# Optimization experiments

Hardware: AMD Instinct MI355X
Metric: run time of the kernel (lower is better)

Reference implementation:

```python
import jax, jax.numpy as jnp
import numpy as np

N, D, V, T = 1024, 64, 32000, 2048
U_DECAY = 0.97
LN_EPS = 1e-6


def _layernorm_row(z):
    # matches torch: (z - mean) / (std_unbiased + eps), std uses ddof=1
    m = z.mean(axis=-1, keepdims=True)
    s = jnp.std(z, axis=-1, ddof=1, keepdims=True)
    return (z - m) / (s + LN_EPS)


def setup_inputs() -> dict:
    key = jax.random.key(0)
    k1, k2, k3, k4, k5 = jax.random.split(key, 5)
    E = jax.random.normal(k1, (D, N), dtype=jnp.float32) / np.float32(np.sqrt(N))
    Dx = jax.random.normal(k2, (N, D), dtype=jnp.float32) / np.float32(np.sqrt(D))
    Dy = jax.random.normal(k3, (N, D), dtype=jnp.float32) / np.float32(np.sqrt(D))
    token_emb = jax.random.normal(k4, (V, D), dtype=jnp.float32) / np.float32(np.sqrt(D))
    tokens = jax.random.randint(k5, (T,), 0, V, dtype=jnp.int32)
    x0 = jnp.zeros((N,), dtype=jnp.float32)
    rho0 = jnp.zeros((D, N), dtype=jnp.float32)
    return {"E": E, "Dx": Dx, "Dy": Dy, "token_emb": token_emb,
            "x0": x0, "rho0": rho0, "tokens": tokens}


def reference(E, Dx, Dy, token_emb, x0, rho0, tokens):
    def step(carry, tok):
        x, rho = carry                        # x: [N], rho: [D, N]
        v_prev = token_emb[tok]               # [D]
        x_t = x + jax.nn.relu(Dx @ v_prev)    # [N], use_relu_lowrank=True
        a_star = rho @ x_t                    # [D]
        y_core = Dy @ _layernorm_row(a_star)  # ln_before_Dy=True -> [N]
        y_t = jax.nn.relu(y_core) * jax.nn.relu(x_t)  # [N]
        v_star = _layernorm_row(E @ y_t)      # [D]
        rho_new = U_DECAY * (rho + jnp.outer(v_prev, x_t))  # [D, N]
        return (x_t, rho_new), (y_t, v_star)

    (_, _), (ys, vs) = jax.lax.scan(step, (x0, rho0), tokens)
    return ys, vs  # [T, N], [T, D]
```

## Files before the change

kernel.cpp:

```cpp
#include <hip/hip_runtime.h>
#include <math.h>

#define NN 1024
#define DD 64
#define TT 2048
#define UDEC 0.97f
#define EPS 1e-6f
#define CC 64
#define NCH 32
#define NSL 8
#define SLW 128
#define C2 32
#define NC2 64

__global__ __launch_bounds__(256) void k_xscan(
    const float* __restrict__ Dx, const float* __restrict__ temb,
    const int* __restrict__ toks, float* __restrict__ Xp, float* __restrict__ S)
{
    const int cs = blockIdx.y;
    const int n  = blockIdx.x * 256 + threadIdx.x;
    __shared__ float Vs[C2][DD];
    for (int i = threadIdx.x; i < C2 * DD; i += 256) {
        int s = i >> 6, d = i & 63;
        Vs[s][d] = temb[toks[cs * C2 + s] * DD + d];
    }
    __syncthreads();
    float dxr[DD];
    const float4* dx4 = reinterpret_cast<const float4*>(Dx + n * DD);
#pragma unroll
    for (int j = 0; j < DD / 4; ++j) {
        float4 v = dx4[j];
        dxr[4*j] = v.x; dxr[4*j+1] = v.y; dxr[4*j+2] = v.z; dxr[4*j+3] = v.w;
    }
    float run = 0.f;
    for (int s = 0; s < C2; ++s) {
        const float4* vr = reinterpret_cast<const float4*>(&Vs[s][0]);
        float a0 = 0.f, a1 = 0.f, a2 = 0.f, a3 = 0.f;
#pragma unroll
        for (int j = 0; j < DD / 4; ++j) {
            float4 v = vr[j];
            a0 += v.x * dxr[4*j];     a1 += v.y * dxr[4*j+1];
            a2 += v.z * dxr[4*j+2];   a3 += v.w * dxr[4*j+3];
        }
        float r = (a0 + a1) + (a2 + a3);
        run += fmaxf(r, 0.f);
        Xp[(cs * C2 + s) * NN + n] = run;
    }
    S[cs * NN + n] = run;
}

__global__ __launch_bounds__(256) void k_base(
    const float* __restrict__ S, const float* __restrict__ x0, float* __restrict__ Bb)
{
    const int n = blockIdx.x * 256 + threadIdx.x;
    float acc = x0[n];
    for (int cs = 0; cs < NC2; ++cs) {
        Bb[cs * NN + n] = acc;
        acc += S[cs * NN + n];
    }
}


__global__ __launch_bounds__(256) void k_M(
    const float* __restrict__ Xp, const float* __restrict__ Bb,
    const float* __restrict__ temb, const int* __restrict__ toks, float* __restrict__ M)
{
    const int c = blockIdx.y, q = blockIdx.x;
    __shared__ float Xs[CC][SLW + 1];
    __shared__ float Vw[CC][DD];
    __shared__ float pw[CC + 1];
    const int tid = threadIdx.x;
    if (tid <= CC) pw[tid] = powf(UDEC, (float)tid);
    __syncthreads();
    for (int i = tid; i < CC * SLW; i += 256) {
        int s = i / SLW, n = i % SLW;
        int t = c * CC + s, gn = q * SLW + n;
        Xs[s][n] = Xp[t * NN + gn] + Bb[(t >> 5) * NN + gn];
    }
    for (int i = tid; i < CC * DD; i += 256) {
        int s = i >> 6, d = i & 63;
        Vw[s][d] = temb[toks[c * CC + s] * DD + d] * pw[CC - s];
    }
    __syncthreads();
    const int n_l = tid & 127;
    const int dh  = tid >> 7;
    float acc[32];
#pragma unroll
    for (int k = 0; k < 32; ++k) acc[k] = 0.f;
    for (int s = 0; s < CC; ++s) {
        float xv = Xs[s][n_l];
        const float4* vr = reinterpret_cast<const float4*>(&Vw[s][dh * 32]);
#pragma unroll
        for (int k8 = 0; k8 < 8; ++k8) {
            float4 v = vr[k8];
            acc[4*k8]   += v.x * xv;  acc[4*k8+1] += v.y * xv;
            acc[4*k8+2] += v.z * xv;  acc[4*k8+3] += v.w * xv;
        }
    }
    for (int k = 0; k < 32; ++k)
        M[(c * DD + dh * 32 + k) * NN + q * SLW + n_l] = acc[k];
}

__global__ __launch_bounds__(256) void k_rho(
    const float* __restrict__ M, const float* __restrict__ rho0, float* __restrict__ Rho)
{
    const int el = blockIdx.x * 256 + threadIdx.x;
    float acc = rho0[el];
    const float uc = powf(UDEC, (float)CC);
    for (int c = 0; c < NCH; ++c) {
        Rho[c * (DD * NN) + el] = acc;
        acc = fmaf(acc, uc, M[c * (DD * NN) + el]);
    }
}

__global__ __launch_bounds__(256) void k_gram(
    const float* __restrict__ Xp, const float* __restrict__ Bb,
    const float* __restrict__ Rho, float* __restrict__ Gp, float* __restrict__ Pp)
{
    const int c = blockIdx.y, q = blockIdx.x;
    __shared__ float Xs[CC][SLW + 1];
    __shared__ float Rs[DD][SLW + 1];
    const int tid = threadIdx.x;
    for (int i = tid; i < CC * SLW; i += 256) {
        int s = i / SLW, n = i % SLW;
        int t = c * CC + s, gn = q * SLW + n;
        Xs[s][n] = Xp[t * NN + gn] + Bb[(t >> 5) * NN + gn];
        Rs[s][n] = Rho[(c * DD + s) * NN + gn];
    }
    __syncthreads();
    const int ti = tid >> 4;
    const int sj = tid & 15;
    float acc[16];
#pragma unroll
    for (int k = 0; k < 16; ++k) acc[k] = 0.f;
    for (int n = 0; n < SLW; ++n) {
        float xt[4], xs[4];
#pragma unroll
        for (int a = 0; a < 4; ++a) xt[a] = Xs[ti * 4 + a][n];
#pragma unroll
        for (int b = 0; b < 4; ++b) xs[b] = Xs[sj * 4 + b][n];
#pragma unroll
        for (int a = 0; a < 4; ++a)
#pragma unroll
            for (int b = 0; b < 4; ++b) acc[a * 4 + b] += xt[a] * xs[b];
    }
    {
        float* base = Gp + ((size_t)(c * NSL + q) * CC) * CC;
#pragma unroll
        for (int a = 0; a < 4; ++a)
            *reinterpret_cast<float4*>(base + (ti * 4 + a) * CC + sj * 4) =
                make_float4(acc[a*4], acc[a*4+1], acc[a*4+2], acc[a*4+3]);
    }
#pragma unroll
    for (int k = 0; k < 16; ++k) acc[k] = 0.f;
    for (int n = 0; n < SLW; ++n) {
        float xt[4], rv[4];
#pragma unroll
        for (int a = 0; a < 4; ++a) xt[a] = Xs[ti * 4 + a][n];
#pragma unroll
        for (int b = 0; b < 4; ++b) rv[b] = Rs[sj * 4 + b][n];
#pragma unroll
        for (int a = 0; a < 4; ++a)
#pragma unroll
            for (int b = 0; b < 4; ++b) acc[a * 4 + b] += xt[a] * rv[b];
    }
    {
        float* base = Pp + ((size_t)(c * NSL + q) * CC) * DD;
#pragma unroll
        for (int a = 0; a < 4; ++a)
            *reinterpret_cast<float4*>(base + (ti * 4 + a) * DD + sj * 4) =
                make_float4(acc[a*4], acc[a*4+1], acc[a*4+2], acc[a*4+3]);
    }
}

__global__ __launch_bounds__(256) void k_astar(
    const float* __restrict__ Gp, const float* __restrict__ Pp,
    const float* __restrict__ temb, const int* __restrict__ toks,
    float* __restrict__ LNA)
{
    const int c = blockIdx.x;
    __shared__ float G[CC][CC + 1];
    __shared__ float P[CC][DD + 1];
    __shared__ float Ve[CC][DD];
    __shared__ float As[CC][DD + 1];
    __shared__ float pw[CC + 1];
    __shared__ float mrow[CC], srow[CC];
    const int tid = threadIdx.x;
    if (tid <= CC) pw[tid] = powf(UDEC, (float)tid);
    for (int i = tid; i < CC * CC; i += 256) {
        int t = i >> 6, s = i & 63;
        float ag = 0.f, ap = 0.f;
#pragma unroll
        for (int qq = 0; qq < NSL; ++qq) {
            ag += Gp[((size_t)(c * NSL + qq) * CC + t) * CC + s];
            ap += Pp[((size_t)(c * NSL + qq) * CC + t) * DD + s];
        }
        G[t][s] = ag; P[t][s] = ap;
    }
    for (int i = tid; i < CC * DD; i += 256) {
        int s = i >> 6, d = i & 63;
        Ve[s][d] = temb[toks[c * CC + s] * DD + d];
    }
    __syncthreads();
    const int t_l = tid >> 2;
    const int qq  = tid & 3;
    float acc[16];
#pragma unroll
    for (int j = 0; j < 16; ++j) acc[j] = pw[t_l] * P[t_l][qq * 16 + j];
    for (int s = 0; s < t_l; ++s) {
        float wv = pw[t_l - s] * G[t_l][s];
        const float4* ver = reinterpret_cast<const float4*>(&Ve[s][qq * 16]);
#pragma unroll
        for (int k = 0; k < 4; ++k) {
            float4 v = ver[k];
            acc[4*k]   += wv * v.x;  acc[4*k+1] += wv * v.y;
            acc[4*k+2] += wv * v.z;  acc[4*k+3] += wv * v.w;
        }
    }
#pragma unroll
    for (int j = 0; j < 16; ++j) As[t_l][qq * 16 + j] = acc[j];
    __syncthreads();
    if (tid < CC) {
        float m = 0.f;
#pragma unroll
        for (int d = 0; d < DD; ++d) m += As[tid][d];
        m *= (1.f / DD);
        float v = 0.f;
#pragma unroll
        for (int d = 0; d < DD; ++d) { float z = As[tid][d] - m; v += z * z; }
        mrow[tid] = m;
        srow[tid] = 1.f / (sqrtf(v / (DD - 1)) + EPS);
    }
    __syncthreads();
    for (int i = tid; i < CC * DD; i += 256) {
        int t = i >> 6, d = i & 63;
        LNA[(c * CC + t) * DD + d] = (As[t][d] - mrow[t]) * srow[t];
    }
}

__global__ __launch_bounds__(256) void k_y(
    const float* __restrict__ LNA, const float* __restrict__ Dy,
    const float* __restrict__ Xp, const float* __restrict__ Bb,
    float* __restrict__ ys)
{
    const int tt = blockIdx.y;
    const int n  = blockIdx.x * 256 + threadIdx.x;
    __shared__ float L[8][DD];
    for (int i = threadIdx.x; i < 8 * DD; i += 256) L[i >> 6][i & 63] = LNA[tt * 8 * DD + i];
    __syncthreads();
    float dyr[DD];
    const float4* dy4 = reinterpret_cast<const float4*>(Dy + n * DD);
#pragma unroll
    for (int j = 0; j < 16; ++j) {
        float4 v = dy4[j];
        dyr[4*j] = v.x; dyr[4*j+1] = v.y; dyr[4*j+2] = v.z; dyr[4*j+3] = v.w;
    }
#pragma unroll
    for (int t = 0; t < 8; ++t) {
        const float4* lr = reinterpret_cast<const float4*>(&L[t][0]);
        float a0 = 0.f, a1 = 0.f, a2 = 0.f, a3 = 0.f;
#pragma unroll
        for (int j = 0; j < 16; ++j) {
            float4 v = lr[j];
            a0 += v.x * dyr[4*j];   a1 += v.y * dyr[4*j+1];
            a2 += v.z * dyr[4*j+2]; a3 += v.w * dyr[4*j+3];
        }
        float yc = (a0 + a1) + (a2 + a3);
        int tg = tt * 8 + t;
        float xv = Xp[tg * NN + n] + Bb[(tg >> 5) * NN + n];
        ys[tg * NN + n] = fmaxf(yc, 0.f) * fmaxf(xv, 0.f);
    }
}

__global__ __launch_bounds__(256) void k_v(
    const float* __restrict__ ys, const float* __restrict__ E, float* __restrict__ vs)
{
    const int tt = blockIdx.x;
    __shared__ float Ys[8][NN];
    __shared__ float pre[8][DD + 1];
    __shared__ float mrow[8], srow[8];
    const int tid = threadIdx.x;
    for (int i = tid; i < 8 * NN; i += 256) Ys[i >> 10][i & 1023] = ys[tt * 8 * NN + i];
    __syncthreads();
    const int d  = tid & 63;
    const int tq = tid >> 6;
    const int t0 = tq * 2;
    const float4* e4 = reinterpret_cast<const float4*>(E + d * NN);
    float a00=0,a01=0,a02=0,a03=0, a10=0,a11=0,a12=0,a13=0;
    for (int j = 0; j < NN / 4; ++j) {
        float4 ev  = e4[j];
        float4 y0v = *reinterpret_cast<const float4*>(&Ys[t0][4 * j]);
        float4 y1v = *reinterpret_cast<const float4*>(&Ys[t0 + 1][4 * j]);
        a00 += ev.x * y0v.x; a01 += ev.y * y0v.y; a02 += ev.z * y0v.z; a03 += ev.w * y0v.w;
        a10 += ev.x * y1v.x; a11 += ev.y * y1v.y; a12 += ev.z * y1v.z; a13 += ev.w * y1v.w;
    }
    pre[t0][d]     = (a00 + a01) + (a02 + a03);
    pre[t0 + 1][d] = (a10 + a11) + (a12 + a13);
    __syncthreads();
    if (tid < 8) {
        float m = 0.f;
#pragma unroll
        for (int dd2 = 0; dd2 < DD; ++dd2) m += pre[tid][dd2];
        m *= (1.f / DD);
        float v = 0.f;
#pragma unroll
        for (int dd2 = 0; dd2 < DD; ++dd2) { float z = pre[tid][dd2] - m; v += z * z; }
        mrow[tid] = m;
        srow[tid] = 1.f / (sqrtf(v / (DD - 1)) + EPS);
    }
    __syncthreads();
    for (int i = tid; i < 8 * DD; i += 256) {
        int t = i >> 6, dd2 = i & 63;
        vs[(tt * 8 + t) * DD + dd2] = (pre[t][dd2] - mrow[t]) * srow[t];
    }
}

extern "C" void kernel_launch(void* const* d_in, const int* in_sizes, int n_in,
                              void* d_out, int out_size, void* d_ws, size_t ws_size,
                              hipStream_t stream) {
    (void)in_sizes; (void)n_in; (void)out_size; (void)ws_size;
    const float* E    = (const float*)d_in[0];
    const float* Dx   = (const float*)d_in[1];
    const float* Dy   = (const float*)d_in[2];
    const float* temb = (const float*)d_in[3];
    const float* x0   = (const float*)d_in[4];
    const float* rho0 = (const float*)d_in[5];
    const int*   toks = (const int*)d_in[6];

    float* ys = (float*)d_out;
    float* vs = ys + (size_t)TT * NN;

    float* w   = (float*)d_ws;
    float* Xp  = w;
    float* S   = Xp  + (size_t)TT * NN;
    float* Bb  = S   + (size_t)NC2 * NN;
    float* M   = Bb  + (size_t)NC2 * NN;
    float* Rho = M   + (size_t)NCH * DD * NN;
    float* LNA = Rho + (size_t)NCH * DD * NN;
    float* Gp = M;
    float* Pp = M + (size_t)NCH * NSL * CC * CC;

    k_xscan<<<dim3(4, NC2),  256, 0, stream>>>(Dx, temb, toks, Xp, S);
    k_base <<<dim3(4),       256, 0, stream>>>(S, x0, Bb);
    k_M    <<<dim3(NSL, NCH),256, 0, stream>>>(Xp, Bb, temb, toks, M);
    k_rho  <<<dim3(DD*NN/256),256,0, stream>>>(M, rho0, Rho);
    k_gram <<<dim3(NSL, NCH),256, 0, stream>>>(Xp, Bb, Rho, Gp, Pp);
    k_astar<<<dim3(NCH),     256, 0, stream>>>(Gp, Pp, temb, toks, LNA);
    k_y    <<<dim3(4, TT/8), 256, 0, stream>>>(LNA, Dy, Xp, Bb, ys);
    k_v    <<<dim3(TT/8),    256, 0, stream>>>(ys, E, vs);
}
```

Baseline: 193.4 us.

## Fuse all phases into one cooperative persistent kernel with grid syncs

Replaces the eight separate kernel launches with one cooperative kernel of 256 blocks that runs each phase in turn, separated by grid-wide barriers. The y and v computations are fused so ys stays in shared memory, the gram phase is split into finer slices with the G and P accumulations merged into one loop, and the a* LayerNorm now uses wave shuffles spread over more blocks. A fallback path launches the phases as separate kernels if the cooperative launch fails. This removes launch gaps and the ys re-read, at the cost of grid.sync overhead and a unified shared-memory footprint that may lower occupancy.

```diff
diff --git a/kernel.cpp b/kernel.cpp
--- a/kernel.cpp
+++ b/kernel.cpp
@@ -1,5 +1,8 @@
 #include <hip/hip_runtime.h>
+#include <hip/hip_cooperative_groups.h>
 #include <math.h>
+
+namespace cg = cooperative_groups;
 
 #define NN 1024
 #define DD 64
@@ -8,78 +11,78 @@
 #define EPS 1e-6f
 #define CC 64
 #define NCH 32
-#define NSL 8
-#define SLW 128
+#define SL3 128
+#define NS5 16
+#define SL5 64
 #define C2 32
 #define NC2 64
 
-__global__ __launch_bounds__(256) void k_xscan(
-    const float* __restrict__ Dx, const float* __restrict__ temb,
-    const int* __restrict__ toks, float* __restrict__ Xp, float* __restrict__ S)
-{
-    const int cs = blockIdx.y;
-    const int n  = blockIdx.x * 256 + threadIdx.x;
-    __shared__ float Vs[C2][DD];
-    for (int i = threadIdx.x; i < C2 * DD; i += 256) {
+struct SP1 { float Vs[C2][DD]; };
+struct SP3 { float Xs[CC][SL3 + 1]; float Vw[CC][DD]; float pw[CC + 1]; };
+struct SP5 { float Xs[CC][SL5 + 1]; float Rs[CC][SL5 + 1]; };
+struct SP6 { float Gs[8][CC + 1]; float Ps[8][DD]; float Ve[CC][DD]; float pw[CC + 1]; };
+struct SP7 { float L[8][DD]; float Ys[8][NN]; float pre[8][DD + 1]; float mrow[8]; float srow[8]; };
+union SMem { SP1 p1; SP3 p3; SP5 p5; SP6 p6; SP7 p7; };
+
+struct KP {
+    const float *E, *Dx, *Dy, *temb, *x0, *rho0;
+    const int* toks;
+    float *ys, *vs;
+    float *Xp, *S, *Bb, *M, *Rho, *Gp, *Pp, *LNA;
+};
+
+__device__ __forceinline__ void phase1(const KP& p, SMem& sm, int bid, int tid) {
+    const int cs = bid >> 2;
+    const int n  = (bid & 3) * 256 + tid;
+    for (int i = tid; i < C2 * DD; i += 256) {
         int s = i >> 6, d = i & 63;
-        Vs[s][d] = temb[toks[cs * C2 + s] * DD + d];
+        sm.p1.Vs[s][d] = p.temb[p.toks[cs * C2 + s] * DD + d];
     }
     __syncthreads();
     float dxr[DD];
-    const float4* dx4 = reinterpret_cast<const float4*>(Dx + n * DD);
-#pragma unroll
-    for (int j = 0; j < DD / 4; ++j) {
+    const float4* dx4 = reinterpret_cast<const float4*>(p.Dx + n * DD);
+#pragma unroll
+    for (int j = 0; j < 16; ++j) {
         float4 v = dx4[j];
         dxr[4*j] = v.x; dxr[4*j+1] = v.y; dxr[4*j+2] = v.z; dxr[4*j+3] = v.w;
     }
     float run = 0.f;
     for (int s = 0; s < C2; ++s) {
-        const float4* vr = reinterpret_cast<const float4*>(&Vs[s][0]);
+        const float4* vr = reinterpret_cast<const float4*>(&sm.p1.Vs[s][0]);
         float a0 = 0.f, a1 = 0.f, a2 = 0.f, a3 = 0.f;
 #pragma unroll
-        for (int j = 0; j < DD / 4; ++j) {
+        for (int j = 0; j < 16; ++j) {
             float4 v = vr[j];
-            a0 += v.x * dxr[4*j];     a1 += v.y * dxr[4*j+1];
-            a2 += v.z * dxr[4*j+2];   a3 += v.w * dxr[4*j+3];
-        }
-        float r = (a0 + a1) + (a2 + a3);
-        run += fmaxf(r, 0.f);
-        Xp[(cs * C2 + s) * NN + n] = run;
-    }
-    S[cs * NN + n] = run;
-}
-
-__global__ __launch_bounds__(256) void k_base(
-    const float* __restrict__ S, const float* __restrict__ x0, float* __restrict__ Bb)
-{
-    const int n = blockIdx.x * 256 + threadIdx.x;
-    float acc = x0[n];
+            a0 += v.x * dxr[4*j];   a1 += v.y * dxr[4*j+1];
+            a2 += v.z * dxr[4*j+2]; a3 += v.w * dxr[4*j+3];
+        }
+        run += fmaxf((a0 + a1) + (a2 + a3), 0.f);
+        p.Xp[(cs * C2 + s) * NN + n] = run;
+    }
+    p.S[cs * NN + n] = run;
+}
+
+__device__ __forceinline__ void phase2(const KP& p, int bid, int tid) {
+    const int n = bid * 256 + tid;
+    float acc = p.x0[n];
     for (int cs = 0; cs < NC2; ++cs) {
-        Bb[cs * NN + n] = acc;
-        acc += S[cs * NN + n];
-    }
-}
-
-
-__global__ __launch_bounds__(256) void k_M(
-    const float* __restrict__ Xp, const float* __restrict__ Bb,
-    const float* __restrict__ temb, const int* __restrict__ toks, float* __restrict__ M)
-{
-    const int c = blockIdx.y, q = blockIdx.x;
-    __shared__ float Xs[CC][SLW + 1];
-    __shared__ float Vw[CC][DD];
-    __shared__ float pw[CC + 1];
-    const int tid = threadIdx.x;
-    if (tid <= CC) pw[tid] = powf(UDEC, (float)tid);
-    __syncthreads();
-    for (int i = tid; i < CC * SLW; i += 256) {
-        int s = i / SLW, n = i % SLW;
-        int t = c * CC + s, gn = q * SLW + n;
-        Xs[s][n] = Xp[t * NN + gn] + Bb[(t >> 5) * NN + gn];
+        p.Bb[cs * NN + n] = acc;
+        acc += p.S[cs * NN + n];
+    }
+}
+
+__device__ __forceinline__ void phase3(const KP& p, SMem& sm, int bid, int tid) {
+    const int c = bid >> 3, q = bid & 7;
+    if (tid <= CC) sm.p3.pw[tid] = powf(UDEC, (float)tid);
+    __syncthreads();
+    for (int i = tid; i < CC * SL3; i += 256) {
+        int s = i / SL3, n = i % SL3;
+        int t = c * CC + s, gn = q * SL3 + n;
+        sm.p3.Xs[s][n] = p.Xp[t * NN + gn] + p.Bb[(t >> 5) * NN + gn];
     }
     for (int i = tid; i < CC * DD; i += 256) {
         int s = i >> 6, d = i & 63;
-        Vw[s][d] = temb[toks[c * CC + s] * DD + d] * pw[CC - s];
+        sm.p3.Vw[s][d] = p.temb[p.toks[c * CC + s] * DD + d] * sm.p3.pw[CC - s];
     }
     __syncthreads();
     const int n_l = tid & 127;
@@ -88,8 +91,8 @@
 #pragma unroll
     for (int k = 0; k < 32; ++k) acc[k] = 0.f;
     for (int s = 0; s < CC; ++s) {
-        float xv = Xs[s][n_l];
-        const float4* vr = reinterpret_cast<const float4*>(&Vw[s][dh * 32]);
+        float xv = sm.p3.Xs[s][n_l];
+        const float4* vr = reinterpret_cast<const float4*>(&sm.p3.Vw[s][dh * 32]);
 #pragma unroll
         for (int k8 = 0; k8 < 8; ++k8) {
             float4 v = vr[k8];
@@ -98,254 +101,234 @@
         }
     }
     for (int k = 0; k < 32; ++k)
-        M[(c * DD + dh * 32 + k) * NN + q * SLW + n_l] = acc[k];
-}
-
-__global__ __launch_bounds__(256) void k_rho(
-    const float* __restrict__ M, const float* __restrict__ rho0, float* __restrict__ Rho)
-{
-    const int el = blockIdx.x * 256 + threadIdx.x;
-    float acc = rho0[el];
+        p.M[(c * DD + dh * 32 + k) * NN + q * SL3 + n_l] = acc[k];
+}
+
+__device__ __forceinline__ void phase4(const KP& p, int bid, int tid) {
+    const int el = bid * 256 + tid;
     const float uc = powf(UDEC, (float)CC);
+    float acc = p.rho0[el];
+#pragma unroll
     for (int c = 0; c < NCH; ++c) {
-        Rho[c * (DD * NN) + el] = acc;
-        acc = fmaf(acc, uc, M[c * (DD * NN) + el]);
-    }
-}
-
-__global__ __launch_bounds__(256) void k_gram(
-    const float* __restrict__ Xp, const float* __restrict__ Bb,
-    const float* __restrict__ Rho, float* __restrict__ Gp, float* __restrict__ Pp)
-{
-    const int c = blockIdx.y, q = blockIdx.x;
-    __shared__ float Xs[CC][SLW + 1];
-    __shared__ float Rs[DD][SLW + 1];
-    const int tid = threadIdx.x;
-    for (int i = tid; i < CC * SLW; i += 256) {
-        int s = i / SLW, n = i % SLW;
-        int t = c * CC + s, gn = q * SLW + n;
-        Xs[s][n] = Xp[t * NN + gn] + Bb[(t >> 5) * NN + gn];
-        Rs[s][n] = Rho[(c * DD + s) * NN + gn];
+        p.Rho[c * (DD * NN) + el] = acc;
+        acc = fmaf(acc, uc, p.M[c * (DD * NN) + el]);
+    }
+}
+
+__device__ __forceinline__ void phase5(const KP& p, SMem& sm, int work, int tid) {
+    const int c = work >> 4, q = work & 15;
+    for (int i = tid; i < CC * SL5; i += 256) {
+        int s = i >> 6, n = i & 63;
+        int t = c * CC + s, gn = q * SL5 + n;
+        sm.p5.Xs[s][n] = p.Xp[t * NN + gn] + p.Bb[(t >> 5) * NN + gn];
+        sm.p5.Rs[s][n] = p.Rho[(c * DD + s) * NN + gn];
     }
     __syncthreads();
     const int ti = tid >> 4;
     const int sj = tid & 15;
-    float acc[16];
-#pragma unroll
-    for (int k = 0; k < 16; ++k) acc[k] = 0.f;
-    for (int n = 0; n < SLW; ++n) {
-        float xt[4], xs[4];
-#pragma unroll
-        for (int a = 0; a < 4; ++a) xt[a] = Xs[ti * 4 + a][n];
-#pragma unroll
-        for (int b = 0; b < 4; ++b) xs[b] = Xs[sj * 4 + b][n];
+    float accG[16], accP[16];
+#pragma unroll
+    for (int k = 0; k < 16; ++k) { accG[k] = 0.f; accP[k] = 0.f; }
+    for (int n = 0; n < SL5; ++n) {
+        float xt[4], xs[4], rv[4];
+#pragma unroll
+        for (int a = 0; a < 4; ++a) xt[a] = sm.p5.Xs[ti * 4 + a][n];
+#pragma unroll
+        for (int b = 0; b < 4; ++b) { xs[b] = sm.p5.Xs[sj * 4 + b][n]; rv[b] = sm.p5.Rs[sj * 4 + b][n]; }
 #pragma unroll
         for (int a = 0; a < 4; ++a)
 #pragma unroll
-            for (int b = 0; b < 4; ++b) acc[a * 4 + b] += xt[a] * xs[b];
-    }
-    {
-        float* base = Gp + ((size_t)(c * NSL + q) * CC) * CC;
-#pragma unroll
-        for (int a = 0; a < 4; ++a)
-            *reinterpret_cast<float4*>(base + (ti * 4 + a) * CC + sj * 4) =
-                make_float4(acc[a*4], acc[a*4+1], acc[a*4+2], acc[a*4+3]);
-    }
-#pragma unroll
-    for (int k = 0; k < 16; ++k) acc[k] = 0.f;
-    for (int n = 0; n < SLW; ++n) {
-        float xt[4], rv[4];
-#pragma unroll
-        for (int a = 0; a < 4; ++a) xt[a] = Xs[ti * 4 + a][n];
-#pragma unroll
-        for (int b = 0; b < 4; ++b) rv[b] = Rs[sj * 4 + b][n];
-#pragma unroll
-        for (int a = 0; a < 4; ++a)
-#pragma unroll
-            for (int b = 0; b < 4; ++b) acc[a * 4 + b] += xt[a] * rv[b];
-    }
-    {
-        float* base = Pp + ((size_t)(c * NSL + q) * CC) * DD;
-#pragma unroll
-        for (int a = 0; a < 4; ++a)
-            *reinterpret_cast<float4*>(base + (ti * 4 + a) * DD + sj * 4) =
-                make_float4(acc[a*4], acc[a*4+1], acc[a*4+2], acc[a*4+3]);
-    }
-}
-
-__global__ __launch_bounds__(256) void k_astar(
-    const float* __restrict__ Gp, const float* __restrict__ Pp,
-    const float* __restrict__ temb, const int* __restrict__ toks,
-    float* __restrict__ LNA)
-{
-    const int c = blockIdx.x;
-    __shared__ float G[CC][CC + 1];
-    __shared__ float P[CC][DD + 1];
-    __shared__ float Ve[CC][DD];
-    __shared__ float As[CC][DD + 1];
-    __shared__ float pw[CC + 1];
-    __shared__ float mrow[CC], srow[CC];
-    const int tid = threadIdx.x;
-    if (tid <= CC) pw[tid] = powf(UDEC, (float)tid);
-    for (int i = tid; i < CC * CC; i += 256) {
-        int t = i >> 6, s = i & 63;
+            for (int b = 0; b < 4; ++b) {
+                accG[a * 4 + b] += xt[a] * xs[b];
+                accP[a * 4 + b] += xt[a] * rv[b];
+            }
+    }
+    float* gbase = p.Gp + ((size_t)(c * NS5 + q) * CC) * CC;
+    float* pbase = p.Pp + ((size_t)(c * NS5 + q) * CC) * DD;
+#pragma unroll
+    for (int a = 0; a < 4; ++a) {
+        *reinterpret_cast<float4*>(gbase + (ti * 4 + a) * CC + sj * 4) =
+            make_float4(accG[a*4], accG[a*4+1], accG[a*4+2], accG[a*4+3]);
+        *reinterpret_cast<float4*>(pbase + (ti * 4 + a) * DD + sj * 4) =
+            make_float4(accP[a*4], accP[a*4+1], accP[a*4+2], accP[a*4+3]);
+    }
+}
+
+__device__ __forceinline__ void phase6(const KP& p, SMem& sm, int bid, int tid) {
+    const int c = bid >> 3, rg = bid & 7;
+    if (tid <= CC) sm.p6.pw[tid] = powf(UDEC, (float)tid);
+    for (int i = tid; i < 8 * CC; i += 256) {
+        int r = i >> 6, s2 = i & 63;
+        int t = rg * 8 + r;
         float ag = 0.f, ap = 0.f;
 #pragma unroll
-        for (int qq = 0; qq < NSL; ++qq) {
-            ag += Gp[((size_t)(c * NSL + qq) * CC + t) * CC + s];
-            ap += Pp[((size_t)(c * NSL + qq) * CC + t) * DD + s];
-        }
-        G[t][s] = ag; P[t][s] = ap;
+        for (int qq = 0; qq < NS5; ++qq) {
+            ag += p.Gp[((size_t)(c * NS5 + qq) * CC + t) * CC + s2];
+            ap += p.Pp[((size_t)(c * NS5 + qq) * CC + t) * DD + s2];
+        }
+        sm.p6.Gs[r][s2] = ag;
+        sm.p6.Ps[r][s2] = ap;
     }
     for (int i = tid; i < CC * DD; i += 256) {
-        int s = i >> 6, d = i & 63;
-        Ve[s][d] = temb[toks[c * CC + s] * DD + d];
-    }
-    __syncthreads();
-    const int t_l = tid >> 2;
-    const int qq  = tid & 3;
-    float acc[16];
-#pragma unroll
-    for (int j = 0; j < 16; ++j) acc[j] = pw[t_l] * P[t_l][qq * 16 + j];
-    for (int s = 0; s < t_l; ++s) {
-        float wv = pw[t_l - s] * G[t_l][s];
-        const float4* ver = reinterpret_cast<const float4*>(&Ve[s][qq * 16]);
-#pragma unroll
-        for (int k = 0; k < 4; ++k) {
-            float4 v = ver[k];
-            acc[4*k]   += wv * v.x;  acc[4*k+1] += wv * v.y;
-            acc[4*k+2] += wv * v.z;  acc[4*k+3] += wv * v.w;
-        }
-    }
-#pragma unroll
-    for (int j = 0; j < 16; ++j) As[t_l][qq * 16 + j] = acc[j];
-    __syncthreads();
-    if (tid < CC) {
-        float m = 0.f;
-#pragma unroll
-        for (int d = 0; d < DD; ++d) m += As[tid][d];
-        m *= (1.f / DD);
-        float v = 0.f;
-#pragma unroll
-        for (int d = 0; d < DD; ++d) { float z = As[tid][d] - m; v += z * z; }
-        mrow[tid] = m;
-        srow[tid] = 1.f / (sqrtf(v / (DD - 1)) + EPS);
-    }
-    __syncthreads();
-    for (int i = tid; i < CC * DD; i += 256) {
-        int t = i >> 6, d = i & 63;
-        LNA[(c * CC + t) * DD + d] = (As[t][d] - mrow[t]) * srow[t];
-    }
-}
-
-__global__ __launch_bounds__(256) void k_y(
-    const float* __restrict__ LNA, const float* __restrict__ Dy,
-    const float* __restrict__ Xp, const float* __restrict__ Bb,
-    float* __restrict__ ys)
-{
-    const int tt = blockIdx.y;
-    const int n  = blockIdx.x * 256 + threadIdx.x;
-    __shared__ float L[8][DD];
-    for (int i = threadIdx.x; i < 8 * DD; i += 256) L[i >> 6][i & 63] = LNA[tt * 8 * DD + i];
-    __syncthreads();
-    float dyr[DD];
-    const float4* dy4 = reinterpret_cast<const float4*>(Dy + n * DD);
-#pragma unroll
-    for (int j = 0; j < 16; ++j) {
-        float4 v = dy4[j];
-        dyr[4*j] = v.x; dyr[4*j+1] = v.y; dyr[4*j+2] = v.z; dyr[4*j+3] = v.w;
-    }
-#pragma unroll
-    for (int t = 0; t < 8; ++t) {
-        const float4* lr = reinterpret_cast<const float4*>(&L[t][0]);
-        float a0 = 0.f, a1 = 0.f, a2 = 0.f, a3 = 0.f;
+        int s2 = i >> 6, d = i & 63;
+        sm.p6.Ve[s2][d] = p.temb[p.toks[c * CC + s2] * DD + d];
+    }
+    __syncthreads();
+    const int r   = tid >> 5;
+    const int dh  = tid & 31;
+    const int t_l = rg * 8 + r;
+    float a0 = sm.p6.pw[t_l] * sm.p6.Ps[r][2 * dh];
+    float a1 = sm.p6.pw[t_l] * sm.p6.Ps[r][2 * dh + 1];
+    for (int s2 = 0; s2 < t_l; ++s2) {
+        float w = sm.p6.pw[t_l - s2] * sm.p6.Gs[r][s2];
+        a0 += w * sm.p6.Ve[s2][2 * dh];
+        a1 += w * sm.p6.Ve[s2][2 * dh + 1];
+    }
+    float ssum = a0 + a1;
+#pragma unroll
+    for (int m = 16; m >= 1; m >>= 1) ssum += __shfl_xor(ssum, m, 64);
+    float mean = ssum * (1.f / DD);
+    float z0 = a0 - mean, z1 = a1 - mean;
+    float vsum = z0 * z0 + z1 * z1;
+#pragma unroll
+    for (int m = 16; m >= 1; m >>= 1) vsum += __shfl_xor(vsum, m, 64);
+    float inv = 1.f / (sqrtf(vsum * (1.f / (DD - 1))) + EPS);
+    int t = c * CC + t_l;
+    *reinterpret_cast<float2*>(&p.LNA[t * DD + 2 * dh]) = make_float2(z0 * inv, z1 * inv);
+}
+
+__device__ __forceinline__ void phase7(const KP& p, SMem& sm, int bid, int tid) {
+    const int t0 = bid * 8;
+    for (int i = tid; i < 8 * DD; i += 256)
+        sm.p7.L[i >> 6][i & 63] = p.LNA[t0 * DD + i];
+    __syncthreads();
+    for (int nq = 0; nq < 4; ++nq) {
+        const int n = nq * 256 + tid;
+        float dyr[DD];
+        const float4* dy4 = reinterpret_cast<const float4*>(p.Dy + n * DD);
 #pragma unroll
         for (int j = 0; j < 16; ++j) {
-            float4 v = lr[j];
-            a0 += v.x * dyr[4*j];   a1 += v.y * dyr[4*j+1];
-            a2 += v.z * dyr[4*j+2]; a3 += v.w * dyr[4*j+3];
-        }
-        float yc = (a0 + a1) + (a2 + a3);
-        int tg = tt * 8 + t;
-        float xv = Xp[tg * NN + n] + Bb[(tg >> 5) * NN + n];
-        ys[tg * NN + n] = fmaxf(yc, 0.f) * fmaxf(xv, 0.f);
-    }
-}
-
-__global__ __launch_bounds__(256) void k_v(
-    const float* __restrict__ ys, const float* __restrict__ E, float* __restrict__ vs)
-{
-    const int tt = blockIdx.x;
-    __shared__ float Ys[8][NN];
-    __shared__ float pre[8][DD + 1];
-    __shared__ float mrow[8], srow[8];
-    const int tid = threadIdx.x;
-    for (int i = tid; i < 8 * NN; i += 256) Ys[i >> 10][i & 1023] = ys[tt * 8 * NN + i];
+            float4 v = dy4[j];
+            dyr[4*j] = v.x; dyr[4*j+1] = v.y; dyr[4*j+2] = v.z; dyr[4*j+3] = v.w;
+        }
+#pragma unroll
+        for (int r = 0; r < 8; ++r) {
+            const float4* lr = reinterpret_cast<const float4*>(&sm.p7.L[r][0]);
+            float a0 = 0.f, a1 = 0.f, a2 = 0.f, a3 = 0.f;
+#pragma unroll
+            for (int j = 0; j < 16; ++j) {
+                float4 v = lr[j];
+                a0 += v.x * dyr[4*j];   a1 += v.y * dyr[4*j+1];
+                a2 += v.z * dyr[4*j+2]; a3 += v.w * dyr[4*j+3];
+            }
+            float yc = (a0 + a1) + (a2 + a3);
+            int t = t0 + r;
+            float xv = p.Xp[t * NN + n] + p.Bb[(t >> 5) * NN + n];
+            float yv = fmaxf(yc, 0.f) * fmaxf(xv, 0.f);
+            p.ys[t * NN + n] = yv;
+            sm.p7.Ys[r][n] = yv;
+        }
+    }
     __syncthreads();
     const int d  = tid & 63;
-    const int tq = tid >> 6;
-    const int t0 = tq * 2;
-    const float4* e4 = reinterpret_cast<const float4*>(E + d * NN);
+    const int r0 = (tid >> 6) * 2;
+    const float4* e4 = reinterpret_cast<const float4*>(p.E + d * NN);
     float a00=0,a01=0,a02=0,a03=0, a10=0,a11=0,a12=0,a13=0;
     for (int j = 0; j < NN / 4; ++j) {
         float4 ev  = e4[j];
-        float4 y0v = *reinterpret_cast<const float4*>(&Ys[t0][4 * j]);
-        float4 y1v = *reinterpret_cast<const float4*>(&Ys[t0 + 1][4 * j]);
+        float4 y0v = *reinterpret_cast<const float4*>(&sm.p7.Ys[r0][4 * j]);
+        float4 y1v = *reinterpret_cast<const float4*>(&sm.p7.Ys[r0 + 1][4 * j]);
         a00 += ev.x * y0v.x; a01 += ev.y * y0v.y; a02 += ev.z * y0v.z; a03 += ev.w * y0v.w;
         a10 += ev.x * y1v.x; a11 += ev.y * y1v.y; a12 += ev.z * y1v.z; a13 += ev.w * y1v.w;
     }
-    pre[t0][d]     = (a00 + a01) + (a02 + a03);
-    pre[t0 + 1][d] = (a10 + a11) + (a12 + a13);
+    sm.p7.pre[r0][d]     = (a00 + a01) + (a02 + a03);
+    sm.p7.pre[r0 + 1][d] = (a10 + a11) + (a12 + a13);
     __syncthreads();
     if (tid < 8) {
         float m = 0.f;
 #pragma unroll
-        for (int dd2 = 0; dd2 < DD; ++dd2) m += pre[tid][dd2];
+        for (int dd2 = 0; dd2 < DD; ++dd2) m += sm.p7.pre[tid][dd2];
         m *= (1.f / DD);
         float v = 0.f;
 #pragma unroll
-        for (int dd2 = 0; dd2 < DD; ++dd2) { float z = pre[tid][dd2] - m; v += z * z; }
-        mrow[tid] = m;
-        srow[tid] = 1.f / (sqrtf(v / (DD - 1)) + EPS);
+        for (int dd2 = 0; dd2 < DD; ++dd2) { float z = sm.p7.pre[tid][dd2] - m; v += z * z; }
+        sm.p7.mrow[tid] = m;
+        sm.p7.srow[tid] = 1.f / (sqrtf(v / (DD - 1)) + EPS);
     }
     __syncthreads();
     for (int i = tid; i < 8 * DD; i += 256) {
-        int t = i >> 6, dd2 = i & 63;
-        vs[(tt * 8 + t) * DD + dd2] = (pre[t][dd2] - mrow[t]) * srow[t];
-    }
-}
+        int r = i >> 6, dd2 = i & 63;
+        p.vs[(t0 + r) * DD + dd2] = (sm.p7.pre[r][dd2] - sm.p7.mrow[r]) * sm.p7.srow[r];
+    }
+}
+
+__global__ __launch_bounds__(256) void fused(KP p) {
+    cg::grid_group grid = cg::this_grid();
+    __shared__ SMem sm;
+    const int tid = threadIdx.x;
+    const int bid = blockIdx.x;
+    phase1(p, sm, bid, tid);
+    grid.sync();
+    if (bid < 4) phase2(p, bid, tid);
+    grid.sync();
+    phase3(p, sm, bid, tid);
+    grid.sync();
+    phase4(p, bid, tid);
+    grid.sync();
+    phase5(p, sm, 2 * bid, tid);
+    __syncthreads();
+    phase5(p, sm, 2 * bid + 1, tid);
+    grid.sync();
+    phase6(p, sm, bid, tid);
+    grid.sync();
+    phase7(p, sm, bid, tid);
+}
+
+__global__ __launch_bounds__(256) void kP1(KP p) { __shared__ SMem sm; phase1(p, sm, blockIdx.x, threadIdx.x); }
+__global__ __launch_bounds__(256) void kP2(KP p) { phase2(p, blockIdx.x, threadIdx.x); }
+__global__ __launch_bounds__(256) void kP3(KP p) { __shared__ SMem sm; phase3(p, sm, blockIdx.x, threadIdx.x); }
+__global__ __launch_bounds__(256) void kP4(KP p) { phase4(p, blockIdx.x, threadIdx.x); }
+__global__ __launch_bounds__(256) void kP5(KP p) { __shared__ SMem sm; phase5(p, sm, blockIdx.x, threadIdx.x); }
+__global__ __launch_bounds__(256) void kP6(KP p) { __shared__ SMem sm; phase6(p, sm, blockIdx.x, threadIdx.x); }
+__global__ __launch_bounds__(256) void kP7(KP p) { __shared__ SMem sm; phase7(p, sm, blockIdx.x, threadIdx.x); }
 
 extern "C" void kernel_launch(void* const* d_in, const int* in_sizes, int n_in,
                               void* d_out, int out_size, void* d_ws, size_t ws_size,
                               hipStream_t stream) {
     (void)in_sizes; (void)n_in; (void)out_size; (void)ws_size;
-    const float* E    = (const float*)d_in[0];
-    const float* Dx   = (const float*)d_in[1];
-    const float* Dy   = (const float*)d_in[2];
-    const float* temb = (const float*)d_in[3];
-    const float* x0   = (const float*)d_in[4];
-    const float* rho0 = (const float*)d_in[5];
-    const int*   toks = (const int*)d_in[6];
-
-    float* ys = (float*)d_out;
-    float* vs = ys + (size_t)TT * NN;
-
-    float* w   = (float*)d_ws;
-    float* Xp  = w;
-    float* S   = Xp  + (size_t)TT * NN;
-    float* Bb  = S   + (size_t)NC2 * NN;
-    float* M   = Bb  + (size_t)NC2 * NN;
-    float* Rho = M   + (size_t)NCH * DD * NN;
-    float* LNA = Rho + (size_t)NCH * DD * NN;
-    float* Gp = M;
-    float* Pp = M + (size_t)NCH * NSL * CC * CC;
-
-    k_xscan<<<dim3(4, NC2),  256, 0, stream>>>(Dx, temb, toks, Xp, S);
-    k_base <<<dim3(4),       256, 0, stream>>>(S, x0, Bb);
-    k_M    <<<dim3(NSL, NCH),256, 0, stream>>>(Xp, Bb, temb, toks, M);
-    k_rho  <<<dim3(DD*NN/256),256,0, stream>>>(M, rho0, Rho);
-    k_gram <<<dim3(NSL, NCH),256, 0, stream>>>(Xp, Bb, Rho, Gp, Pp);
-    k_astar<<<dim3(NCH),     256, 0, stream>>>(Gp, Pp, temb, toks, LNA);
-    k_y    <<<dim3(4, TT/8), 256, 0, stream>>>(LNA, Dy, Xp, Bb, ys);
-    k_v    <<<dim3(TT/8),    256, 0, stream>>>(ys, E, vs);
-}
+    KP p;
+    p.E    = (const float*)d_in[0];
+    p.Dx   = (const float*)d_in[1];
+    p.Dy   = (const float*)d_in[2];
+    p.temb = (const float*)d_in[3];
+    p.x0   = (const float*)d_in[4];
+    p.rho0 = (const float*)d_in[5];
+    p.toks = (const int*)d_in[6];
+
+    p.ys = (float*)d_out;
+    p.vs = p.ys + (size_t)TT * NN;
+
+    float* w = (float*)d_ws;
+    p.Xp  = w;
+    p.S   = p.Xp  + (size_t)TT * NN;
+    p.Bb  = p.S   + (size_t)NC2 * NN;
+    p.M   = p.Bb  + (size_t)NC2 * NN;
+    p.Rho = p.M   + (size_t)NCH * DD * NN;
+    p.Gp  = p.Rho + (size_t)NCH * DD * NN;
+    p.Pp  = p.Gp  + (size_t)NCH * NS5 * CC * CC;
+    p.LNA = p.Pp  + (size_t)NCH * NS5 * CC * DD;
+
+    void* args[] = { &p };
+    hipError_t err = hipLaunchCooperativeKernel((const void*)fused, dim3(256), dim3(256),
+                                                args, 0, stream);
+    if (err != hipSuccess) {
+        (void)hipGetLastError();
+        kP1<<<dim3(256), 256, 0, stream>>>(p);
+        kP2<<<dim3(4),   256, 0, stream>>>(p);
+        kP3<<<dim3(256), 256, 0, stream>>>(p);
+        kP4<<<dim3(256), 256, 0, stream>>>(p);
+        kP5<<<dim3(512), 256, 0, stream>>>(p);
+        kP6<<<dim3(256), 256, 0, stream>>>(p);
+        kP7<<<dim3(256), 256, 0, stream>>>(p);
+    }
+}
```

Measured after the change: 403.2 us. +108.4%, slower.
